# Kernel tuning notes

Hardware: AMD Instinct MI355X
Metric: run time of the kernel (lower is better)

Reference implementation:

```python
import jax, jax.numpy as jnp
import numpy as np

TAU = 0.1
MASK_VAL = 1e9


def setup_inputs() -> dict:
    key = jax.random.key(0)
    ka, kb = jax.random.split(key)
    B, D = 4096, 512
    return {
        "view_a": jax.random.normal(ka, (B, D), dtype=jnp.float32),
        "view_b": jax.random.normal(kb, (B, D), dtype=jnp.float32),
    }


def _l2norm(x):
    return x / jnp.maximum(jnp.linalg.norm(x, axis=-1, keepdims=True), 1e-12)


def reference(view_a, view_b):
    a = _l2norm(view_a)
    b = _l2norm(view_b)
    B = a.shape[0]
    labels = jnp.arange(B)  # start_i = 0 (single device)
    mask = jnp.eye(B, dtype=a.dtype) * MASK_VAL

    logits_aa = a @ a.T / TAU - mask
    logits_bb = b @ b.T / TAU - mask
    logits_ab = a @ b.T / TAU
    logits_ba = b @ a.T / TAU

    full_a = jnp.concatenate([logits_ab, logits_aa], axis=1)  # [B, 2B]
    full_b = jnp.concatenate([logits_ba, logits_bb], axis=1)

    def ce(logits):
        logp = jax.nn.log_softmax(logits, axis=-1)
        return -jnp.mean(jnp.take_along_axis(logp, labels[:, None], axis=-1))

    loss = (ce(full_a) + ce(full_b)) / 2

    pred = jnp.argmax(full_a, axis=-1)
    acc = 100.0 * jnp.sum(pred == labels) / B
    return loss, acc
```

## Files before the change

kernel.cpp:

```cpp
#include <hip/hip_runtime.h>
#include <stdint.h>


#define BN 4096
#define DK 512
#define NSPLIT 16
#define NEG_BIG -1e30f
#define SCL 0.15625f
#define TILE_BYTES (64 * DK)

typedef __attribute__((ext_vector_type(16))) float floatx16;

__device__ __forceinline__ void mlmerge(float& m, float& l, float m2, float l2) {
  float mn = fmaxf(m, m2);
  l = l * __expf(m - mn) + l2 * __expf(m2 - mn);
  m = mn;
}

__global__ void __launch_bounds__(256) prep_kernel(
    const float* __restrict__ A, const float* __restrict__ Bv,
    unsigned char* __restrict__ An, unsigned char* __restrict__ Bn,
    float* __restrict__ diag, float* __restrict__ out) {
  if (blockIdx.x == 0 && threadIdx.x < 2) out[threadIdx.x] = 0.0f;
  const int w = threadIdx.x >> 6, lane = threadIdx.x & 63;
  const int row = blockIdx.x * 4 + w;
  const float4* pa4 = (const float4*)(A + (size_t)row * DK);
  const float4* pb4 = (const float4*)(Bv + (size_t)row * DK);
  float4 a0 = pa4[lane * 2], a1 = pa4[lane * 2 + 1];
  float4 b0 = pb4[lane * 2], b1 = pb4[lane * 2 + 1];
  float ssa = a0.x * a0.x + a0.y * a0.y + a0.z * a0.z + a0.w * a0.w +
              a1.x * a1.x + a1.y * a1.y + a1.z * a1.z + a1.w * a1.w;
  float ssb = b0.x * b0.x + b0.y * b0.y + b0.z * b0.z + b0.w * b0.w +
              b1.x * b1.x + b1.y * b1.y + b1.z * b1.z + b1.w * b1.w;
  float sab = a0.x * b0.x + a0.y * b0.y + a0.z * b0.z + a0.w * b0.w +
              a1.x * b1.x + a1.y * b1.y + a1.z * b1.z + a1.w * b1.w;
#pragma unroll
  for (int off = 32; off > 0; off >>= 1) {
    ssa += __shfl_xor(ssa, off);
    ssb += __shfl_xor(ssb, off);
    sab += __shfl_xor(sab, off);
  }
  float na = fmaxf(sqrtf(ssa), 1e-12f);
  float nb = fmaxf(sqrtf(ssb), 1e-12f);
  const float s = 8.0f;
  float sa = s / na, sb = s / nb;
  const int doff = (lane >> 2) * 32 + (lane & 1) * 16 + ((lane >> 1) & 1) * 8;
  {
    int v0 = __builtin_amdgcn_cvt_pk_fp8_f32(a0.x * sa, a0.y * sa, 0, false);
    v0 = __builtin_amdgcn_cvt_pk_fp8_f32(a0.z * sa, a0.w * sa, v0, true);
    int v1 = __builtin_amdgcn_cvt_pk_fp8_f32(a1.x * sa, a1.y * sa, 0, false);
    v1 = __builtin_amdgcn_cvt_pk_fp8_f32(a1.z * sa, a1.w * sa, v1, true);
    int2 pv; pv.x = v0; pv.y = v1;
    *(int2*)(An + (size_t)row * DK + doff) = pv;
  }
  {
    int v0 = __builtin_amdgcn_cvt_pk_fp8_f32(b0.x * sb, b0.y * sb, 0, false);
    v0 = __builtin_amdgcn_cvt_pk_fp8_f32(b0.z * sb, b0.w * sb, v0, true);
    int v1 = __builtin_amdgcn_cvt_pk_fp8_f32(b1.x * sb, b1.y * sb, 0, false);
    v1 = __builtin_amdgcn_cvt_pk_fp8_f32(b1.z * sb, b1.w * sb, v1, true);
    int2 pv; pv.x = v0; pv.y = v1;
    *(int2*)(Bn + (size_t)row * DK + doff) = pv;
  }
  if (lane == 0) diag[row] = (sab / (na * nb)) * 10.0f;
}

__global__ void __launch_bounds__(256, 2) tiles_kernel(
    const unsigned char* __restrict__ An, const unsigned char* __restrict__ Bn,
    float* __restrict__ pmA, float* __restrict__ plA,
    float* __restrict__ pmB, float* __restrict__ plB) {
  __shared__ __align__(16) unsigned char smem[2 * TILE_BYTES];

  const int rb = blockIdx.x;
  const int split = blockIdx.y;
  const int tid = threadIdx.x;
  const int lane = tid & 63, w = tid >> 6;
  const int n5 = lane & 31, h = lane >> 5;
  const int r0 = rb * 128;
  const int myrow = r0 + w * 32 + n5;

  long af[32];
  auto loadfrags = [&](const unsigned char* base) {
    const unsigned char* p = base + (size_t)myrow * DK + h * 16;
#pragma unroll
    for (int kc2 = 0; kc2 < 16; ++kc2) {
      long2 v = *(const long2*)(p + kc2 * 32);
      af[2 * kc2] = v.x; af[2 * kc2 + 1] = v.y;
    }
  };

  float m[16], l[16];
#pragma unroll
  for (int r = 0; r < 16; ++r) { m[r] = NEG_BIG; l[r] = 0.f; }

  auto flush = [&](float* pm, float* pl) {
#pragma unroll
    for (int off = 1; off < 32; off <<= 1)
#pragma unroll
      for (int r = 0; r < 16; ++r) {
        float mo = __shfl_xor(m[r], off), lo = __shfl_xor(l[r], off);
        mlmerge(m[r], l[r], mo, lo);
      }
    if (n5 == 0) {
      const int base = split * BN;
#pragma unroll
      for (int r = 0; r < 16; ++r) {
        const int row = r0 + w * 32 + (r & 3) + 8 * (r >> 2) + 4 * h;
        pm[base + row] = m[r];
        pl[base + row] = l[r];
      }
    }
#pragma unroll
    for (int r = 0; r < 16; ++r) { m[r] = NEG_BIG; l[r] = 0.f; }
  };

  auto stage = [&](unsigned char* buf, int jt) {
    const unsigned char* csrc = (jt < 64) ? An : Bn;
    const int cb = (jt & 63) * 64;
#pragma unroll
    for (int ii = 0; ii < 8; ++ii) {
      const int cp = w * 8 + ii;
      const int cl = cp * 2 + h;
      const unsigned char* src =
          csrc + (size_t)(cb + cl) * DK + ((n5 ^ (cl & 7)) * 16);
      __builtin_amdgcn_global_load_lds(
          (const __attribute__((address_space(1))) void*)src,
          (__attribute__((address_space(3))) void*)(buf + cp * 1024),
          16, 0, 0);
    }
  };

  stage(smem, split * 8);
  loadfrags(An);
  __syncthreads();

  for (int u = 0; u < 16; ++u) {
    const int t = u & 7;
    const int jt = split * 8 + t;
    unsigned char* cur = smem + (u & 1) * TILE_BYTES;
    unsigned char* nxt = smem + ((u + 1) & 1) * TILE_BYTES;
    if (u < 15) stage(nxt, split * 8 + ((t + 1) & 7));
    if (u == 8) {
      flush(pmA, plA);
      loadfrags(Bn);
    }

    floatx16 acc[2];
#pragma unroll
    for (int cs = 0; cs < 2; ++cs)
#pragma unroll
      for (int r = 0; r < 16; ++r) acc[cs][r] = 0.f;

    const unsigned char* bbase = cur + (size_t)n5 * DK;
#pragma unroll
    for (int kc2 = 0; kc2 < 16; ++kc2) {
      const int chunk = ((2 * kc2 + h) ^ (n5 & 7)) * 16;
#pragma unroll
      for (int cs = 0; cs < 2; ++cs) {
        long2 bv = *(const long2*)(bbase + cs * 32 * DK + chunk);
        acc[cs] = __builtin_amdgcn_mfma_f32_32x32x16_fp8_fp8(af[2 * kc2], bv.x, acc[cs], 0, 0, 0);
        acc[cs] = __builtin_amdgcn_mfma_f32_32x32x16_fp8_fp8(af[2 * kc2 + 1], bv.y, acc[cs], 0, 0, 0);
      }
    }

    const bool dtile = (((jt & 63) >> 1) == rb);
    const int colbase = (jt & 63) * 64;
#pragma unroll
    for (int r = 0; r < 16; ++r) {
      const int rowg = r0 + w * 32 + (r & 3) + 8 * (r >> 2) + 4 * h;
      float v0 = acc[0][r] * SCL, v1 = acc[1][r] * SCL;
      if (dtile) {
        if (rowg == colbase + n5)      v0 = NEG_BIG;
        if (rowg == colbase + 32 + n5) v1 = NEG_BIG;
      }
      float mn = fmaxf(m[r], fmaxf(v0, v1));
      l[r] = l[r] * __expf(m[r] - mn) + __expf(v0 - mn) + __expf(v1 - mn);
      m[r] = mn;
    }
    __syncthreads();
  }

  flush(pmB, plB);
}

__global__ void __launch_bounds__(256) finalize_kernel(
    const float* __restrict__ pmA, const float* __restrict__ plA,
    const float* __restrict__ pmB, const float* __restrict__ plB,
    const float* __restrict__ diag, float* __restrict__ out) {
  const int row = blockIdx.x * 256 + threadIdx.x;
  float Ma = NEG_BIG, La = 0.f, Mb = NEG_BIG, Lb = 0.f;
#pragma unroll
  for (int s = 0; s < NSPLIT; ++s) {
    mlmerge(Ma, La, pmA[s * BN + row], plA[s * BN + row]);
    mlmerge(Mb, Lb, pmB[s * BN + row], plB[s * BN + row]);
  }
  const float d = diag[row];
  float corr = (d >= Ma) ? 1.f : 0.f;
  float mna = fmaxf(Ma, d);
  float lseA = mna + logf(La * __expf(Ma - mna) + __expf(d - mna));
  float mnb = fmaxf(Mb, d);
  float lseB = mnb + logf(Lb * __expf(Mb - mnb) + __expf(d - mnb));
  float lossi = (lseA - d) + (lseB - d);
#pragma unroll
  for (int off = 32; off > 0; off >>= 1) {
    lossi += __shfl_xor(lossi, off);
    corr += __shfl_xor(corr, off);
  }
  __shared__ float sred[2][4];
  if ((threadIdx.x & 63) == 0) {
    int w = threadIdx.x >> 6;
    sred[0][w] = lossi; sred[1][w] = corr;
  }
  __syncthreads();
  if (threadIdx.x == 0) {
    float ls = sred[0][0] + sred[0][1] + sred[0][2] + sred[0][3];
    float cs = sred[1][0] + sred[1][1] + sred[1][2] + sred[1][3];
    atomicAdd(&out[0], ls * (1.0f / 8192.0f));
    atomicAdd(&out[1], cs * (100.0f / 4096.0f));
  }
}

extern "C" void kernel_launch(void* const* d_in, const int* in_sizes, int n_in,
                              void* d_out, int out_size, void* d_ws, size_t ws_size,
                              hipStream_t stream) {
  const float* A = (const float*)d_in[0];
  const float* Bv = (const float*)d_in[1];
  unsigned char* An = (unsigned char*)d_ws;
  unsigned char* Bn = An + (size_t)BN * DK;
  float* diag = (float*)(Bn + (size_t)BN * DK);
  float* pmA = diag + BN;
  float* plA = pmA + NSPLIT * BN;
  float* pmB = plA + NSPLIT * BN;
  float* plB = pmB + NSPLIT * BN;
  float* out = (float*)d_out;

  prep_kernel<<<BN / 4, 256, 0, stream>>>(A, Bv, An, Bn, diag, out);
  tiles_kernel<<<dim3(32, 16), 256, 0, stream>>>(An, Bn, pmA, plA, pmB, plB);
  finalize_kernel<<<BN / 256, 256, 0, stream>>>(pmA, plA, pmB, plB, diag, out);
}
```

Before: 135.4 us.

## Use fixed-offset softmax sums with atomics and fold finalize into last block

```diff
diff --git a/kernel.cpp b/kernel.cpp
--- a/kernel.cpp
+++ b/kernel.cpp
@@ -4,24 +4,20 @@
 
 #define BN 4096
 #define DK 512
-#define NSPLIT 16
 #define NEG_BIG -1e30f
 #define SCL 0.15625f
 #define TILE_BYTES (64 * DK)
 
 typedef __attribute__((ext_vector_type(16))) float floatx16;
 
-__device__ __forceinline__ void mlmerge(float& m, float& l, float m2, float l2) {
-  float mn = fmaxf(m, m2);
-  l = l * __expf(m - mn) + l2 * __expf(m2 - mn);
-  m = mn;
-}
-
 __global__ void __launch_bounds__(256) prep_kernel(
     const float* __restrict__ A, const float* __restrict__ Bv,
     unsigned char* __restrict__ An, unsigned char* __restrict__ Bn,
-    float* __restrict__ diag, float* __restrict__ out) {
-  if (blockIdx.x == 0 && threadIdx.x < 2) out[threadIdx.x] = 0.0f;
+    float* __restrict__ diag, float* __restrict__ zero_region) {
+  {
+    const int idx = blockIdx.x * 256 + threadIdx.x;
+    if (idx < 3 * BN + 1) zero_region[idx] = 0.0f;
+  }
   const int w = threadIdx.x >> 6, lane = threadIdx.x & 63;
   const int row = blockIdx.x * 4 + w;
   const float4* pa4 = (const float4*)(A + (size_t)row * DK);
@@ -66,8 +62,10 @@
 
 __global__ void __launch_bounds__(256, 2) tiles_kernel(
     const unsigned char* __restrict__ An, const unsigned char* __restrict__ Bn,
-    float* __restrict__ pmA, float* __restrict__ plA,
-    float* __restrict__ pmB, float* __restrict__ plB) {
+    const float* __restrict__ diag,
+    float* __restrict__ accLA, float* __restrict__ accLB,
+    unsigned* __restrict__ accMA, unsigned* __restrict__ cnt,
+    float* __restrict__ out) {
   __shared__ __align__(16) unsigned char smem[2 * TILE_BYTES];
 
   const int rb = blockIdx.x;
@@ -88,29 +86,29 @@
     }
   };
 
-  float m[16], l[16];
-#pragma unroll
-  for (int r = 0; r < 16; ++r) { m[r] = NEG_BIG; l[r] = 0.f; }
-
-  auto flush = [&](float* pm, float* pl) {
+  float l[16], mx[16];
+#pragma unroll
+  for (int r = 0; r < 16; ++r) { l[r] = 0.f; mx[r] = NEG_BIG; }
+
+  auto flush = [&](float* accL, bool doMax) {
 #pragma unroll
     for (int off = 1; off < 32; off <<= 1)
 #pragma unroll
       for (int r = 0; r < 16; ++r) {
-        float mo = __shfl_xor(m[r], off), lo = __shfl_xor(l[r], off);
-        mlmerge(m[r], l[r], mo, lo);
+        l[r] += __shfl_xor(l[r], off);
+        if (doMax) mx[r] = fmaxf(mx[r], __shfl_xor(mx[r], off));
       }
     if (n5 == 0) {
-      const int base = split * BN;
 #pragma unroll
       for (int r = 0; r < 16; ++r) {
         const int row = r0 + w * 32 + (r & 3) + 8 * (r >> 2) + 4 * h;
-        pm[base + row] = m[r];
-        pl[base + row] = l[r];
-      }
-    }
-#pragma unroll
-    for (int r = 0; r < 16; ++r) { m[r] = NEG_BIG; l[r] = 0.f; }
+        atomicAdd(&accL[row], l[r]);
+        if (doMax)
+          atomicMax(&accMA[row], __float_as_uint(mx[r] * SCL + 20.0f));
+      }
+    }
+#pragma unroll
+    for (int r = 0; r < 16; ++r) { l[r] = 0.f; mx[r] = NEG_BIG; }
   };
 
   auto stage = [&](unsigned char* buf, int jt) {
@@ -140,7 +138,7 @@
     unsigned char* nxt = smem + ((u + 1) & 1) * TILE_BYTES;
     if (u < 15) stage(nxt, split * 8 + ((t + 1) & 7));
     if (u == 8) {
-      flush(pmA, plA);
+      flush(accLA, true);
       loadfrags(Bn);
     }
 
@@ -164,58 +162,57 @@
 
     const bool dtile = (((jt & 63) >> 1) == rb);
     const int colbase = (jt & 63) * 64;
+    const bool passA = (u < 8);
 #pragma unroll
     for (int r = 0; r < 16; ++r) {
-      const int rowg = r0 + w * 32 + (r & 3) + 8 * (r >> 2) + 4 * h;
-      float v0 = acc[0][r] * SCL, v1 = acc[1][r] * SCL;
+      float v0 = acc[0][r], v1 = acc[1][r];
       if (dtile) {
+        const int rowg = r0 + w * 32 + (r & 3) + 8 * (r >> 2) + 4 * h;
         if (rowg == colbase + n5)      v0 = NEG_BIG;
         if (rowg == colbase + 32 + n5) v1 = NEG_BIG;
       }
-      float mn = fmaxf(m[r], fmaxf(v0, v1));
-      l[r] = l[r] * __expf(m[r] - mn) + __expf(v0 - mn) + __expf(v1 - mn);
-      m[r] = mn;
+      if (passA) mx[r] = fmaxf(mx[r], fmaxf(v0, v1));
+      l[r] += __expf(v0 * SCL - 10.0f) + __expf(v1 * SCL - 10.0f);
     }
     __syncthreads();
   }
-
-  flush(pmB, plB);
-}
-
-__global__ void __launch_bounds__(256) finalize_kernel(
-    const float* __restrict__ pmA, const float* __restrict__ plA,
-    const float* __restrict__ pmB, const float* __restrict__ plB,
-    const float* __restrict__ diag, float* __restrict__ out) {
-  const int row = blockIdx.x * 256 + threadIdx.x;
-  float Ma = NEG_BIG, La = 0.f, Mb = NEG_BIG, Lb = 0.f;
-#pragma unroll
-  for (int s = 0; s < NSPLIT; ++s) {
-    mlmerge(Ma, La, pmA[s * BN + row], plA[s * BN + row]);
-    mlmerge(Mb, Lb, pmB[s * BN + row], plB[s * BN + row]);
-  }
-  const float d = diag[row];
-  float corr = (d >= Ma) ? 1.f : 0.f;
-  float mna = fmaxf(Ma, d);
-  float lseA = mna + logf(La * __expf(Ma - mna) + __expf(d - mna));
-  float mnb = fmaxf(Mb, d);
-  float lseB = mnb + logf(Lb * __expf(Mb - mnb) + __expf(d - mnb));
-  float lossi = (lseA - d) + (lseB - d);
-#pragma unroll
-  for (int off = 32; off > 0; off >>= 1) {
-    lossi += __shfl_xor(lossi, off);
-    corr += __shfl_xor(corr, off);
-  }
-  __shared__ float sred[2][4];
-  if ((threadIdx.x & 63) == 0) {
-    int w = threadIdx.x >> 6;
-    sred[0][w] = lossi; sred[1][w] = corr;
-  }
+  flush(accLB, false);
+
   __syncthreads();
-  if (threadIdx.x == 0) {
-    float ls = sred[0][0] + sred[0][1] + sred[0][2] + sred[0][3];
-    float cs = sred[1][0] + sred[1][1] + sred[1][2] + sred[1][3];
-    atomicAdd(&out[0], ls * (1.0f / 8192.0f));
-    atomicAdd(&out[1], cs * (100.0f / 4096.0f));
+  unsigned* flag = (unsigned*)smem;
+  if (tid == 0) {
+    __threadfence();
+    unsigned old = atomicAdd(cnt, 1u);
+    *flag = (old == gridDim.x * gridDim.y - 1) ? 1u : 0u;
+  }
+  __syncthreads();
+  if (*flag) {
+    __threadfence();
+    float lsum = 0.f, csum = 0.f;
+#pragma unroll
+    for (int i = 0; i < 16; ++i) {
+      const int row = tid + i * 256;
+      float La = accLA[row], Lb = accLB[row];
+      float Mu = __uint_as_float(accMA[row]) - 20.0f;
+      float d = diag[row];
+      float e = __expf(d - 10.0f);
+      lsum += (20.0f + logf(La + e) + logf(Lb + e)) - 2.0f * d;
+      csum += (d >= Mu) ? 1.f : 0.f;
+    }
+#pragma unroll
+    for (int off = 32; off > 0; off >>= 1) {
+      lsum += __shfl_xor(lsum, off);
+      csum += __shfl_xor(csum, off);
+    }
+    float* red = (float*)(smem + 64);
+    if (lane == 0) { red[w * 2] = lsum; red[w * 2 + 1] = csum; }
+    __syncthreads();
+    if (tid == 0) {
+      float L = red[0] + red[2] + red[4] + red[6];
+      float C = red[1] + red[3] + red[5] + red[7];
+      out[0] = L * (1.0f / 8192.0f);
+      out[1] = C * (100.0f / 4096.0f);
+    }
   }
 }
 
@@ -227,13 +224,13 @@
   unsigned char* An = (unsigned char*)d_ws;
   unsigned char* Bn = An + (size_t)BN * DK;
   float* diag = (float*)(Bn + (size_t)BN * DK);
-  float* pmA = diag + BN;
-  float* plA = pmA + NSPLIT * BN;
-  float* pmB = plA + NSPLIT * BN;
-  float* plB = pmB + NSPLIT * BN;
+  float* accLA = diag + BN;
+  float* accLB = accLA + BN;
+  unsigned* accMA = (unsigned*)(accLB + BN);
+  unsigned* cnt = accMA + BN;
   float* out = (float*)d_out;
 
-  prep_kernel<<<BN / 4, 256, 0, stream>>>(A, Bv, An, Bn, diag, out);
-  tiles_kernel<<<dim3(32, 16), 256, 0, stream>>>(An, Bn, pmA, plA, pmB, plB);
-  finalize_kernel<<<BN / 256, 256, 0, stream>>>(pmA, plA, pmB, plB, diag, out);
+  prep_kernel<<<BN / 4, 256, 0, stream>>>(A, Bv, An, Bn, diag, accLA);
+  tiles_kernel<<<dim3(32, 16), 256, 0, stream>>>(An, Bn, diag, accLA, accLB,
+                                                 accMA, cnt, out);
 }
```

Measured after the change: 142.4 us. +5.1%, slower.

## Use fixed-max softmax with exp2 and 32x32x64 scaled FP8 MFMA

Applied to the files above, without the earlier changes.

```diff
diff --git a/kernel.cpp b/kernel.cpp
--- a/kernel.cpp
+++ b/kernel.cpp
@@ -7,15 +7,12 @@
 #define NSPLIT 16
 #define NEG_BIG -1e30f
 #define SCL 0.15625f
+#define SCL2 0.225396744f
+#define C2 14.4269504f
 #define TILE_BYTES (64 * DK)
 
 typedef __attribute__((ext_vector_type(16))) float floatx16;
-
-__device__ __forceinline__ void mlmerge(float& m, float& l, float m2, float l2) {
-  float mn = fmaxf(m, m2);
-  l = l * __expf(m - mn) + l2 * __expf(m2 - mn);
-  m = mn;
-}
+typedef __attribute__((ext_vector_type(8))) int intx8;
 
 __global__ void __launch_bounds__(256) prep_kernel(
     const float* __restrict__ A, const float* __restrict__ Bv,
@@ -66,8 +63,7 @@
 
 __global__ void __launch_bounds__(256, 2) tiles_kernel(
     const unsigned char* __restrict__ An, const unsigned char* __restrict__ Bn,
-    float* __restrict__ pmA, float* __restrict__ plA,
-    float* __restrict__ pmB, float* __restrict__ plB) {
+    float* __restrict__ pSA, float* __restrict__ pMA, float* __restrict__ pSB) {
   __shared__ __align__(16) unsigned char smem[2 * TILE_BYTES];
 
   const int rb = blockIdx.x;
@@ -78,40 +74,21 @@
   const int r0 = rb * 128;
   const int myrow = r0 + w * 32 + n5;
 
-  long af[32];
+  intx8 aw[8];
   auto loadfrags = [&](const unsigned char* base) {
     const unsigned char* p = base + (size_t)myrow * DK + h * 16;
 #pragma unroll
-    for (int kc2 = 0; kc2 < 16; ++kc2) {
-      long2 v = *(const long2*)(p + kc2 * 32);
-      af[2 * kc2] = v.x; af[2 * kc2 + 1] = v.y;
+    for (int i = 0; i < 8; ++i) {
+      int4 c0 = *(const int4*)(p + i * 64);
+      int4 c1 = *(const int4*)(p + i * 64 + 32);
+      intx8 v = {c0.x, c0.y, c0.z, c0.w, c1.x, c1.y, c1.z, c1.w};
+      aw[i] = v;
     }
   };
 
-  float m[16], l[16];
-#pragma unroll
-  for (int r = 0; r < 16; ++r) { m[r] = NEG_BIG; l[r] = 0.f; }
-
-  auto flush = [&](float* pm, float* pl) {
-#pragma unroll
-    for (int off = 1; off < 32; off <<= 1)
-#pragma unroll
-      for (int r = 0; r < 16; ++r) {
-        float mo = __shfl_xor(m[r], off), lo = __shfl_xor(l[r], off);
-        mlmerge(m[r], l[r], mo, lo);
-      }
-    if (n5 == 0) {
-      const int base = split * BN;
-#pragma unroll
-      for (int r = 0; r < 16; ++r) {
-        const int row = r0 + w * 32 + (r & 3) + 8 * (r >> 2) + 4 * h;
-        pm[base + row] = m[r];
-        pl[base + row] = l[r];
-      }
-    }
-#pragma unroll
-    for (int r = 0; r < 16; ++r) { m[r] = NEG_BIG; l[r] = 0.f; }
-  };
+  float l[16], mx[16];
+#pragma unroll
+  for (int r = 0; r < 16; ++r) { l[r] = 0.f; mx[r] = NEG_BIG; }
 
   auto stage = [&](unsigned char* buf, int jt) {
     const unsigned char* csrc = (jt < 64) ? An : Bn;
@@ -133,16 +110,13 @@
   loadfrags(An);
   __syncthreads();
 
+  const int swz = n5 & 7;
   for (int u = 0; u < 16; ++u) {
     const int t = u & 7;
     const int jt = split * 8 + t;
     unsigned char* cur = smem + (u & 1) * TILE_BYTES;
     unsigned char* nxt = smem + ((u + 1) & 1) * TILE_BYTES;
     if (u < 15) stage(nxt, split * 8 + ((t + 1) & 7));
-    if (u == 8) {
-      flush(pmA, plA);
-      loadfrags(Bn);
-    }
 
     floatx16 acc[2];
 #pragma unroll
@@ -152,54 +126,88 @@
 
     const unsigned char* bbase = cur + (size_t)n5 * DK;
 #pragma unroll
-    for (int kc2 = 0; kc2 < 16; ++kc2) {
-      const int chunk = ((2 * kc2 + h) ^ (n5 & 7)) * 16;
+    for (int i = 0; i < 8; ++i) {
+      const int p1 = ((4 * i + h) ^ swz) * 16;
+      const int p2 = ((4 * i + 2 + h) ^ swz) * 16;
 #pragma unroll
       for (int cs = 0; cs < 2; ++cs) {
-        long2 bv = *(const long2*)(bbase + cs * 32 * DK + chunk);
-        acc[cs] = __builtin_amdgcn_mfma_f32_32x32x16_fp8_fp8(af[2 * kc2], bv.x, acc[cs], 0, 0, 0);
-        acc[cs] = __builtin_amdgcn_mfma_f32_32x32x16_fp8_fp8(af[2 * kc2 + 1], bv.y, acc[cs], 0, 0, 0);
+        int4 b0 = *(const int4*)(bbase + cs * 32 * DK + p1);
+        int4 b1 = *(const int4*)(bbase + cs * 32 * DK + p2);
+        intx8 bw = {b0.x, b0.y, b0.z, b0.w, b1.x, b1.y, b1.z, b1.w};
+        acc[cs] = __builtin_amdgcn_mfma_scale_f32_32x32x64_f8f6f4(
+            aw[i], bw, acc[cs], 0, 0, 0, 0x7F7F7F7F, 0, 0x7F7F7F7F);
       }
     }
 
     const bool dtile = (((jt & 63) >> 1) == rb);
     const int colbase = (jt & 63) * 64;
+    const bool passA = (u < 8);
 #pragma unroll
     for (int r = 0; r < 16; ++r) {
-      const int rowg = r0 + w * 32 + (r & 3) + 8 * (r >> 2) + 4 * h;
-      float v0 = acc[0][r] * SCL, v1 = acc[1][r] * SCL;
+      float v0 = acc[0][r], v1 = acc[1][r];
       if (dtile) {
+        const int rowg = r0 + w * 32 + (r & 3) + 8 * (r >> 2) + 4 * h;
         if (rowg == colbase + n5)      v0 = NEG_BIG;
         if (rowg == colbase + 32 + n5) v1 = NEG_BIG;
       }
-      float mn = fmaxf(m[r], fmaxf(v0, v1));
-      l[r] = l[r] * __expf(m[r] - mn) + __expf(v0 - mn) + __expf(v1 - mn);
-      m[r] = mn;
+      if (passA) mx[r] = fmaxf(mx[r], fmaxf(v0, v1));
+      l[r] += exp2f(fmaf(v0, SCL2, -C2)) + exp2f(fmaf(v1, SCL2, -C2));
+    }
+
+    if (u == 7) {
+#pragma unroll
+      for (int off = 1; off < 32; off <<= 1)
+#pragma unroll
+        for (int r = 0; r < 16; ++r) {
+          l[r] += __shfl_xor(l[r], off);
+          mx[r] = fmaxf(mx[r], __shfl_xor(mx[r], off));
+        }
+      if (n5 == 0) {
+#pragma unroll
+        for (int r = 0; r < 16; ++r) {
+          const int row = r0 + w * 32 + (r & 3) + 8 * (r >> 2) + 4 * h;
+          pSA[split * BN + row] = l[r];
+          pMA[split * BN + row] = mx[r] * SCL;
+        }
+      }
+#pragma unroll
+      for (int r = 0; r < 16; ++r) l[r] = 0.f;
+      loadfrags(Bn);
     }
     __syncthreads();
   }
 
-  flush(pmB, plB);
+#pragma unroll
+  for (int off = 1; off < 32; off <<= 1)
+#pragma unroll
+    for (int r = 0; r < 16; ++r) l[r] += __shfl_xor(l[r], off);
+  if (n5 == 0) {
+#pragma unroll
+    for (int r = 0; r < 16; ++r) {
+      const int row = r0 + w * 32 + (r & 3) + 8 * (r >> 2) + 4 * h;
+      pSB[split * BN + row] = l[r];
+    }
+  }
 }
 
 __global__ void __launch_bounds__(256) finalize_kernel(
-    const float* __restrict__ pmA, const float* __restrict__ plA,
-    const float* __restrict__ pmB, const float* __restrict__ plB,
-    const float* __restrict__ diag, float* __restrict__ out) {
+    const float* __restrict__ pSA, const float* __restrict__ pMA,
+    const float* __restrict__ pSB, const float* __restrict__ diag,
+    float* __restrict__ out) {
   const int row = blockIdx.x * 256 + threadIdx.x;
-  float Ma = NEG_BIG, La = 0.f, Mb = NEG_BIG, Lb = 0.f;
+  float SA = 0.f, SB = 0.f, MA = NEG_BIG;
 #pragma unroll
   for (int s = 0; s < NSPLIT; ++s) {
-    mlmerge(Ma, La, pmA[s * BN + row], plA[s * BN + row]);
-    mlmerge(Mb, Lb, pmB[s * BN + row], plB[s * BN + row]);
+    SA += pSA[s * BN + row];
+    SB += pSB[s * BN + row];
+    MA = fmaxf(MA, pMA[s * BN + row]);
   }
   const float d = diag[row];
-  float corr = (d >= Ma) ? 1.f : 0.f;
-  float mna = fmaxf(Ma, d);
-  float lseA = mna + logf(La * __expf(Ma - mna) + __expf(d - mna));
-  float mnb = fmaxf(Mb, d);
-  float lseB = mnb + logf(Lb * __expf(Mb - mnb) + __expf(d - mnb));
+  const float eL = exp2f(fmaf(d, 1.44269504f, -C2));
+  float lseA = 10.0f + logf(SA + eL);
+  float lseB = 10.0f + logf(SB + eL);
   float lossi = (lseA - d) + (lseB - d);
+  float corr = (d >= MA) ? 1.f : 0.f;
 #pragma unroll
   for (int off = 32; off > 0; off >>= 1) {
     lossi += __shfl_xor(lossi, off);
@@ -227,13 +235,12 @@
   unsigned char* An = (unsigned char*)d_ws;
   unsigned char* Bn = An + (size_t)BN * DK;
   float* diag = (float*)(Bn + (size_t)BN * DK);
-  float* pmA = diag + BN;
-  float* plA = pmA + NSPLIT * BN;
-  float* pmB = plA + NSPLIT * BN;
-  float* plB = pmB + NSPLIT * BN;
+  float* pSA = diag + BN;
+  float* pMA = pSA + NSPLIT * BN;
+  float* pSB = pMA + NSPLIT * BN;
   float* out = (float*)d_out;
 
   prep_kernel<<<BN / 4, 256, 0, stream>>>(A, Bv, An, Bn, diag, out);
-  tiles_kernel<<<dim3(32, 16), 256, 0, stream>>>(An, Bn, pmA, plA, pmB, plB);
-  finalize_kernel<<<BN / 256, 256, 0, stream>>>(pmA, plA, pmB, plB, diag, out);
-}
+  tiles_kernel<<<dim3(32, 16), 256, 0, stream>>>(An, Bn, pSA, pMA, pSB);
+  finalize_kernel<<<BN / 256, 256, 0, stream>>>(pSA, pMA, pSB, diag, out);
+}
```

New measurement: 123.0 us. -9.2%, faster.
